# Kernel optimization log

Measured on AMD Instinct MI355X. Metric: run time of the kernel, lower is better.

Reference implementation:

```python
import jax, jax.numpy as jnp
import numpy as np
from jax import lax

EPS = 1e-12
ALPHA = 20.0
TEMP = 10.0
TAU = 0.45
LAMBDA_N = 0.3
REP_W = 0.15
MOMENTUM = 0.9
N_SINK_ITER = 3


def _norm(x):
    # F.normalize(p=2, dim=1, eps=1e-12)
    return x / jnp.maximum(jnp.linalg.norm(x, axis=-1, keepdims=True), EPS)


def sinkhorn(sim, alpha=ALPHA, n_iterations=N_SINK_ITER):
    Q = jnp.exp(alpha * sim).T  # [K, B]
    K, B = Q.shape
    Q = Q / jnp.sum(Q)
    for _ in range(n_iterations):
        Q = Q / (jnp.sum(Q, axis=1, keepdims=True) * K)
        Q = Q / (jnp.sum(Q, axis=0, keepdims=True) * B)
    return (Q * B).T  # [B, K]


def update_negative_centers(n_feats, positive_center, negative_centers):
    # all under no_grad in the original
    nf = _norm(n_feats)
    pos = _norm(positive_center)
    sim_to_pos = (nf @ pos.T)[:, 0]                       # [Nn]
    keep = sim_to_pos < 0.7
    negc = _norm(negative_centers)
    sim = nf @ negc.T                                     # [Nn, K]
    assign = jnp.argmax(sim, axis=1)
    K = negative_centers.shape[0]
    onehot = jax.nn.one_hot(assign, K, dtype=n_feats.dtype) * keep[:, None].astype(n_feats.dtype)
    counts = jnp.sum(onehot, axis=0)                      # [K]
    sums = onehot.T @ n_feats                             # [K, D] masked per-cluster sums of raw feats
    means = sums / jnp.maximum(counts[:, None], 1.0)
    new_center = _norm(means)
    lerped = negative_centers + (new_center - negative_centers) * (1.0 - MOMENTUM)
    lerped = lerped / jnp.maximum(jnp.linalg.norm(lerped, axis=1, keepdims=True), EPS)
    # update only clusters with >=3 assigned kept features (skips everything if keep.sum()==0)
    return jnp.where((counts >= 3.0)[:, None], lerped, negative_centers)


def setup_inputs() -> dict:
    key = jax.random.key(0)
    ks = jax.random.split(key, 6)
    dim, n_proxies, n_centers = 512, 1024, 4
    return {
        'p_feats': jax.random.normal(ks[0], (16384, dim), jnp.float32),
        'u_feats': jax.random.normal(ks[1], (65536, dim), jnp.float32),
        'n_feats': jax.random.normal(ks[2], (32768, dim), jnp.float32),
        'positive_center': _norm(jax.random.normal(ks[3], (1, dim), jnp.float32)),
        'proxy_u': jax.random.normal(ks[4], (n_proxies, dim), jnp.float32),
        'negative_centers': _norm(jax.random.normal(ks[5], (n_centers, dim), jnp.float32)),
    }


def reference(p_feats, u_feats, n_feats, positive_center, proxy_u, negative_centers):
    pos = lax.stop_gradient(positive_center)   # requires_grad=False param
    negc0 = lax.stop_gradient(negative_centers)  # buffer

    # l_loss: mean(1 - cos(pos, p_feats))
    dist = _norm(pos) @ _norm(p_feats).T       # [1, Np]
    l_loss = jnp.mean(1.0 - dist)

    # EMA update of negative centers (no_grad)
    negc = lax.stop_gradient(update_negative_centers(lax.stop_gradient(n_feats), pos, negc0))

    # n branch: self-distillation on negative centers
    sim_n = _norm(n_feats) @ _norm(negc).T     # [Nn, K]
    target_n = jax.nn.softmax(sim_n, axis=1)
    loss_n = -jnp.mean(jnp.sum(target_n * jax.nn.log_softmax(sim_n, axis=1), axis=1))

    # pseudo-label branch on u_feats vs negative centers (sinkhorn targets, detached)
    sim_u_neg = _norm(u_feats) @ _norm(negc).T  # [Nu, K]
    soft_assign = sinkhorn(lax.stop_gradient(sim_u_neg))
    loss_pseudo = -jnp.mean(jnp.sum(soft_assign * jax.nn.log_softmax(sim_u_neg, axis=1), axis=1))

    n_loss = (loss_n + loss_pseudo) / 2.0

    # u branch vs learnable proxies
    u_similarity = _norm(u_feats) @ _norm(proxy_u).T  # [Nu, P]
    u_target = sinkhorn(lax.stop_gradient(u_similarity))
    u_loss = -jnp.mean(jnp.sum(u_target * jax.nn.log_softmax(u_similarity * TEMP, axis=1), axis=1))

    # repulsion
    sim_np = (_norm(negc) @ _norm(pos).T)[:, 0]       # [K]
    rep_np = -jnp.mean(jnp.log(jnp.clip(1.0 - sim_np, 1e-6, None)))
    nc = _norm(negc)
    sim_nn = nc @ nc.T                                 # [K, K]
    K = negc.shape[0]
    offdiag = ~jnp.eye(K, dtype=bool)
    logs = jnp.where(offdiag, jnp.log(jnp.clip(1.0 - sim_nn, 1e-6, None)), 0.0)
    rep_nn = -jnp.sum(logs) / (K * K - K)
    repulsion_loss = rep_np + 0.1 * rep_nn

    cls_loss = TAU * l_loss + LAMBDA_N * n_loss + (0.55 - TAU) * u_loss + REP_W * repulsion_loss
    return cls_loss, l_loss, u_loss, n_loss, repulsion_loss
```

## Files before the change

kernel.cpp:

```cpp
#include <hip/hip_runtime.h>
#include <hip/hip_bf16.h>

typedef __attribute__((ext_vector_type(8))) short short8;
typedef __attribute__((ext_vector_type(8))) unsigned short ushort8;
typedef __attribute__((ext_vector_type(4))) float f32x4;

#define EPSN 1e-12f
#define GN 1024
#define GK 512

__device__ __forceinline__ float bf2f(unsigned short h) {
  union { unsigned int u; float f; } c; c.u = ((unsigned int)h) << 16; return c.f;
}
__device__ __forceinline__ unsigned short f2bf(float f) {
  union { float f; unsigned int u; } c; c.f = f;
  unsigned int u = c.u;
  return (unsigned short)((u + 0x7fffu + ((u >> 16) & 1u)) >> 16);
}
__device__ __forceinline__ float wredsum(float v) {
  v += __shfl_xor(v, 32); v += __shfl_xor(v, 16); v += __shfl_xor(v, 8);
  v += __shfl_xor(v, 4);  v += __shfl_xor(v, 2);  v += __shfl_xor(v, 1);
  return v;
}

#define GLL(g, l) __builtin_amdgcn_global_load_lds( \
    (const __attribute__((address_space(1))) unsigned int*)(g), \
    (__attribute__((address_space(3))) unsigned int*)(l), 16, 0, 0)

__global__ void k_prep(const float* __restrict__ pc, const float* __restrict__ nc,
                       float* __restrict__ pos_hat, float* __restrict__ negc0_hat) {
  int tid = threadIdx.x, lane = tid & 63, w = tid >> 6;
  const float* src = (w == 0) ? pc : (nc + (w - 1) * 512);
  float* dst = (w == 0) ? pos_hat : (negc0_hat + (w - 1) * 512);
  float4 a = *(const float4*)(src + lane * 8);
  float4 b = *(const float4*)(src + lane * 8 + 4);
  float x[8] = {a.x,a.y,a.z,a.w,b.x,b.y,b.z,b.w};
  float ss = 0.f;
  #pragma unroll
  for (int j = 0; j < 8; j++) ss += x[j]*x[j];
  ss = wredsum(ss);
  float inv = 1.f / fmaxf(sqrtf(ss), EPSN);
  #pragma unroll
  for (int j = 0; j < 8; j++) dst[lane*8+j] = x[j]*inv;
}

__global__ __launch_bounds__(256) void k_redcol(const float* __restrict__ P, float* __restrict__ R,
                                                int nrows, int ncols) {
  __shared__ float lred[64];
  int tid = threadIdx.x, lane = tid & 63, w = tid >> 6;
  int colg = blockIdx.x * 16;
  int ci = tid & 15;
  int r0 = tid >> 4;
  float s = 0.f;
  for (int r = r0; r < nrows; r += 16)
    s += P[(size_t)r * ncols + colg + ci];
  s += __shfl_xor(s, 16); s += __shfl_xor(s, 32);
  if (lane < 16) lred[w * 16 + lane] = s;
  __syncthreads();
  if (tid < 16) R[colg + tid] = lred[tid] + lred[16 + tid] + lred[32 + tid] + lred[48 + tid];
}

__global__ __launch_bounds__(256) void k_rownormP(const float* __restrict__ X,
                                                  unsigned short* __restrict__ Y,
                                                  float* __restrict__ invn, int rows) {
  int lane = threadIdx.x & 63;
  int w0 = blockIdx.x * 4 + (threadIdx.x >> 6);
  int nw = gridDim.x * 4;
  for (int row = w0; row < rows; row += nw) {
    const float* src = X + (size_t)row * 512 + lane * 8;
    float4 a = *(const float4*)src;
    float4 b = *(const float4*)(src + 4);
    float x[8] = {a.x,a.y,a.z,a.w,b.x,b.y,b.z,b.w};
    float ss = 0.f;
    #pragma unroll
    for (int j = 0; j < 8; j++) ss += x[j]*x[j];
    ss = wredsum(ss);
    float inv = 1.f / fmaxf(sqrtf(ss), EPSN);
    if (lane == 0) invn[row] = inv;
    ushort8 o;
    #pragma unroll
    for (int j = 0; j < 8; j++) o[j] = f2bf(x[j]);
    *(ushort8*)(Y + (size_t)row * 512 + lane * 8) = o;
  }
}

__global__ __launch_bounds__(256) void k_plns(const float* __restrict__ PF, const float* __restrict__ ph_g,
                                              float* __restrict__ PlossP,
                                              const float* __restrict__ NF, const float* __restrict__ nch0,
                                              float* __restrict__ inv_n, float* __restrict__ CntP,
                                              float* __restrict__ SumP) {
  __shared__ float fl[8192];
  __shared__ float cb[16];
  int tid = threadIdx.x, lane = tid & 63, w = tid >> 6;
  if (blockIdx.x < 512) {
    float ph[8];
    #pragma unroll
    for (int j = 0; j < 8; j++) ph[j] = ph_g[lane*8+j];
    float lsum = 0.f;
    int row0 = blockIdx.x * 32;
    for (int rr = w; rr < 32; rr += 4) {
      int row = row0 + rr;
      const float* src = PF + (size_t)row * 512 + lane * 8;
      float4 a = *(const float4*)src;
      float4 b = *(const float4*)(src + 4);
      float x[8] = {a.x,a.y,a.z,a.w,b.x,b.y,b.z,b.w};
      float ss = 0.f, dp = 0.f;
      #pragma unroll
      for (int j = 0; j < 8; j++) { ss += x[j]*x[j]; dp += x[j]*ph[j]; }
      ss = wredsum(ss); dp = wredsum(dp);
      if (lane == 0) lsum += dp / fmaxf(sqrtf(ss), EPSN);
    }
    if (lane == 0) cb[w] = lsum;
    __syncthreads();
    if (tid == 0) PlossP[blockIdx.x] = cb[0]+cb[1]+cb[2]+cb[3];
    return;
  }
  const int nb = blockIdx.x - 512;
  float ph[8], nh[4][8];
  #pragma unroll
  for (int j = 0; j < 8; j++) ph[j] = ph_g[lane*8+j];
  #pragma unroll
  for (int c = 0; c < 4; c++)
    #pragma unroll
    for (int j = 0; j < 8; j++) nh[c][j] = nch0[c*512 + lane*8 + j];
  float acc[4][8];
  float cnt[4] = {0.f,0.f,0.f,0.f};
  #pragma unroll
  for (int c = 0; c < 4; c++)
    #pragma unroll
    for (int j = 0; j < 8; j++) acc[c][j] = 0.f;
  int row0 = nb * 32;
  for (int rr = w; rr < 32; rr += 4) {
    int row = row0 + rr;
    const float* src = NF + (size_t)row * 512 + lane * 8;
    float4 a = *(const float4*)src;
    float4 b = *(const float4*)(src + 4);
    float x[8] = {a.x,a.y,a.z,a.w,b.x,b.y,b.z,b.w};
    float ss = 0.f, dp = 0.f, dn[4] = {0.f,0.f,0.f,0.f};
    #pragma unroll
    for (int j = 0; j < 8; j++) {
      ss += x[j]*x[j]; dp += x[j]*ph[j];
      #pragma unroll
      for (int c = 0; c < 4; c++) dn[c] += x[j]*nh[c][j];
    }
    ss = wredsum(ss); dp = wredsum(dp);
    #pragma unroll
    for (int c = 0; c < 4; c++) dn[c] = wredsum(dn[c]);
    float inv = 1.f / fmaxf(sqrtf(ss), EPSN);
    if (lane == 0) inv_n[row] = inv;
    float sp = dp * inv;
    float s0 = dn[0]*inv, s1 = dn[1]*inv, s2 = dn[2]*inv, s3 = dn[3]*inv;
    int am = 0; float best = s0;
    if (s1 > best) { best = s1; am = 1; }
    if (s2 > best) { best = s2; am = 2; }
    if (s3 > best) { best = s3; am = 3; }
    float kf = (sp < 0.7f) ? 1.f : 0.f;
    #pragma unroll
    for (int c = 0; c < 4; c++) {
      float m = (am == c) ? kf : 0.f;
      #pragma unroll
      for (int j = 0; j < 8; j++) acc[c][j] += m * x[j];
      if (lane == 0) cnt[c] += m;
    }
  }
  #pragma unroll
  for (int c = 0; c < 4; c++)
    #pragma unroll
    for (int j = 0; j < 8; j++) fl[w*2048 + c*512 + lane*8 + j] = acc[c][j];
  if (lane == 0) {
    #pragma unroll
    for (int c = 0; c < 4; c++) cb[w*4+c] = cnt[c];
  }
  __syncthreads();
  for (int q = tid; q < 2048; q += 256)
    SumP[(size_t)nb * 2048 + q] = fl[q] + fl[2048+q] + fl[4096+q] + fl[6144+q];
  if (tid < 4) CntP[nb * 4 + tid] = cb[tid] + cb[4+tid] + cb[8+tid] + cb[12+tid];
}

__global__ void k_center(const float* __restrict__ CntP, const float* __restrict__ sums,
                         const float* __restrict__ negc_raw, const float* __restrict__ pos_hat,
                         float* __restrict__ negc_hat, float* __restrict__ scal) {
  __shared__ float hbuf[2048];
  __shared__ float spn[4];
  __shared__ float snn[16];
  int tid = threadIdx.x, lane = tid & 63, c = tid >> 6;
  float cs = 0.f;
  for (int r = lane; r < 1024; r += 64) cs += CntP[r*4 + c];
  float cnt = wredsum(cs);
  float x[8], raw[8], ph[8];
  #pragma unroll
  for (int j = 0; j < 8; j++) {
    x[j] = sums[c*512 + lane*8 + j] / fmaxf(cnt, 1.f);
    raw[j] = negc_raw[c*512 + lane*8 + j];
    ph[j] = pos_hat[lane*8 + j];
  }
  float ss = 0.f;
  #pragma unroll
  for (int j = 0; j < 8; j++) ss += x[j]*x[j];
  ss = wredsum(ss);
  float n1 = fmaxf(sqrtf(ss), EPSN);
  #pragma unroll
  for (int j = 0; j < 8; j++) x[j] = raw[j] + (x[j]/n1 - raw[j]) * 0.1f;
  ss = 0.f;
  #pragma unroll
  for (int j = 0; j < 8; j++) ss += x[j]*x[j];
  ss = wredsum(ss);
  float n2 = fmaxf(sqrtf(ss), EPSN);
  bool upd = (cnt >= 3.0f);
  #pragma unroll
  for (int j = 0; j < 8; j++) x[j] = upd ? (x[j]/n2) : raw[j];
  ss = 0.f;
  #pragma unroll
  for (int j = 0; j < 8; j++) ss += x[j]*x[j];
  ss = wredsum(ss);
  float n3 = fmaxf(sqrtf(ss), EPSN);
  float dp = 0.f;
  #pragma unroll
  for (int j = 0; j < 8; j++) {
    x[j] = x[j] / n3;
    negc_hat[c*512 + lane*8 + j] = x[j];
    hbuf[c*512 + lane*8 + j] = x[j];
    dp += x[j] * ph[j];
  }
  dp = wredsum(dp);
  if (lane == 0) spn[c] = dp;
  __syncthreads();
  float d4[4] = {0.f,0.f,0.f,0.f};
  #pragma unroll
  for (int c2 = 0; c2 < 4; c2++) {
    float d = 0.f;
    #pragma unroll
    for (int j = 0; j < 8; j++) d += x[j] * hbuf[c2*512 + lane*8 + j];
    d4[c2] = wredsum(d);
  }
  if (lane == 0) {
    #pragma unroll
    for (int c2 = 0; c2 < 4; c2++) snn[c*4 + c2] = d4[c2];
  }
  __syncthreads();
  if (tid == 0) {
    float rep_np = 0.f;
    for (int i = 0; i < 4; i++) rep_np += logf(fmaxf(1.f - spn[i], 1e-6f));
    rep_np = -rep_np * 0.25f;
    float rep_nn = 0.f;
    for (int i = 0; i < 4; i++)
      for (int j2 = 0; j2 < 4; j2++)
        if (i != j2) rep_nn += logf(fmaxf(1.f - snn[i*4+j2], 1e-6f));
    rep_nn = -rep_nn / 12.f;
    scal[4] = rep_np + 0.1f * rep_nn;
  }
}

__global__ __launch_bounds__(256) void k_nlup(const float* __restrict__ NF, const float* __restrict__ inv_n,
                                              const float* __restrict__ nch, float* __restrict__ NlossP,
                                              const float* __restrict__ U, float* __restrict__ SU,
                                              float* __restrict__ UPp, unsigned short* __restrict__ Uh,
                                              float* __restrict__ invU) {
  __shared__ float sh[16];
  int tid = threadIdx.x, lane = tid & 63, w = tid >> 6;
  float nh[4][8];
  #pragma unroll
  for (int c = 0; c < 4; c++)
    #pragma unroll
    for (int j = 0; j < 8; j++) nh[c][j] = nch[c*512 + lane*8 + j];
  if (blockIdx.x < 1024) {
    float lsum = 0.f;
    int row0 = blockIdx.x * 32;
    for (int rr = w; rr < 32; rr += 4) {
      int row = row0 + rr;
      const float* src = NF + (size_t)row * 512 + lane * 8;
      float4 a = *(const float4*)src;
      float4 b = *(const float4*)(src + 4);
      float x[8] = {a.x,a.y,a.z,a.w,b.x,b.y,b.z,b.w};
      float dn[4] = {0.f,0.f,0.f,0.f};
      #pragma unroll
      for (int j = 0; j < 8; j++)
        #pragma unroll
        for (int c = 0; c < 4; c++) dn[c] += x[j]*nh[c][j];
      #pragma unroll
      for (int c = 0; c < 4; c++) dn[c] = wredsum(dn[c]);
      if (lane == 0) {
        float inv = inv_n[row];
        float s0 = dn[0]*inv, s1 = dn[1]*inv, s2 = dn[2]*inv, s3 = dn[3]*inv;
        float mx = fmaxf(fmaxf(s0,s1), fmaxf(s2,s3));
        float e0 = __expf(s0-mx), e1 = __expf(s1-mx), e2 = __expf(s2-mx), e3 = __expf(s3-mx);
        float Z = e0+e1+e2+e3;
        lsum += (mx + logf(Z)) - (e0*s0+e1*s1+e2*s2+e3*s3)/Z;
      }
    }
    if (lane == 0) sh[w] = lsum;
    __syncthreads();
    if (tid == 0) NlossP[blockIdx.x] = sh[0]+sh[1]+sh[2]+sh[3];
    return;
  }
  const int ub = blockIdx.x - 1024;
  float eacc[4] = {0.f,0.f,0.f,0.f};
  int row0 = ub * 32;
  for (int rr = w; rr < 32; rr += 4) {
    int row = row0 + rr;
    const float* src = U + (size_t)row * 512 + lane * 8;
    float4 a = *(const float4*)src;
    float4 b = *(const float4*)(src + 4);
    float x[8] = {a.x,a.y,a.z,a.w,b.x,b.y,b.z,b.w};
    float ss = 0.f, dn[4] = {0.f,0.f,0.f,0.f};
    #pragma unroll
    for (int j = 0; j < 8; j++) {
      ss += x[j]*x[j];
      #pragma unroll
      for (int c = 0; c < 4; c++) dn[c] += x[j]*nh[c][j];
    }
    ss = wredsum(ss);
    #pragma unroll
    for (int c = 0; c < 4; c++) dn[c] = wredsum(dn[c]);
    float inv = 1.f / fmaxf(sqrtf(ss), EPSN);
    ushort8 o;
    #pragma unroll
    for (int j = 0; j < 8; j++) o[j] = f2bf(x[j]);
    *(ushort8*)(Uh + (size_t)row * 512 + lane * 8) = o;
    if (lane == 0) {
      invU[row] = inv;
      float4 sv; sv.x = dn[0]*inv; sv.y = dn[1]*inv; sv.z = dn[2]*inv; sv.w = dn[3]*inv;
      *(float4*)(SU + (size_t)row * 4) = sv;
      eacc[0] += __expf(20.f*sv.x); eacc[1] += __expf(20.f*sv.y);
      eacc[2] += __expf(20.f*sv.z); eacc[3] += __expf(20.f*sv.w);
    }
  }
  if (lane == 0) {
    #pragma unroll
    for (int c = 0; c < 4; c++) sh[w*4+c] = eacc[c];
  }
  __syncthreads();
  if (tid < 4) UPp[ub * 4 + tid] = sh[tid] + sh[4+tid] + sh[8+tid] + sh[12+tid];
}

__global__ __launch_bounds__(256) void k_psink(const float* __restrict__ SU, const float* __restrict__ Pin,
                                               int n_in, float* __restrict__ Pout,
                                               float* __restrict__ PLout, int mode) {
  __shared__ float lr[16];
  int tid = threadIdx.x, lane = tid & 63, w = tid >> 6;
  float i0 = 0.f, i1 = 0.f, i2 = 0.f, i3 = 0.f;
  for (int r = tid; r < n_in; r += 256) {
    float4 v = *(const float4*)(Pin + (size_t)r * 4);
    i0 += v.x; i1 += v.y; i2 += v.z; i3 += v.w;
  }
  i0 = wredsum(i0); i1 = wredsum(i1); i2 = wredsum(i2); i3 = wredsum(i3);
  if (lane == 0) { lr[w*4+0] = i0; lr[w*4+1] = i1; lr[w*4+2] = i2; lr[w*4+3] = i3; }
  __syncthreads();
  float R0 = lr[0]+lr[4]+lr[8]+lr[12];
  float R1_ = lr[1]+lr[5]+lr[9]+lr[13];
  float R2_ = lr[2]+lr[6]+lr[10]+lr[14];
  float R3_ = lr[3]+lr[7]+lr[11]+lr[15];
  float r0 = 1.f/(4.f*R0), r1 = 1.f/(4.f*R1_), r2 = 1.f/(4.f*R2_), r3 = 1.f/(4.f*R3_);
  float a0 = 0.f, a1 = 0.f, a2 = 0.f, a3 = 0.f, lsum = 0.f;
  int row = blockIdx.x * blockDim.x + threadIdx.x;
  {
    float4 s = *(const float4*)(SU + (size_t)row * 4);
    float x0 = __expf(20.f*s.x), x1 = __expf(20.f*s.y);
    float x2 = __expf(20.f*s.z), x3 = __expf(20.f*s.w);
    float E0 = x0*r0, E1 = x1*r1, E2 = x2*r2, E3 = x3*r3;
    float cf = 1.f / ((E0+E1+E2+E3) * 65536.f);
    if (mode == 1) { a0 = x0*cf; a1 = x1*cf; a2 = x2*cf; a3 = x3*cf; }
    else {
      float term = (E0*s.x + E1*s.y + E2*s.z + E3*s.w) * 65536.f * cf;
      float mx = fmaxf(fmaxf(s.x,s.y), fmaxf(s.z,s.w));
      float z = __expf(s.x-mx)+__expf(s.y-mx)+__expf(s.z-mx)+__expf(s.w-mx);
      lsum = (mx + logf(z)) - term;
    }
  }
  __syncthreads();
  if (mode == 1) {
    a0 = wredsum(a0); a1 = wredsum(a1); a2 = wredsum(a2); a3 = wredsum(a3);
    if (lane == 0) { lr[w*4+0] = a0; lr[w*4+1] = a1; lr[w*4+2] = a2; lr[w*4+3] = a3; }
    __syncthreads();
    if (tid < 4) Pout[blockIdx.x * 4 + tid] = lr[tid] + lr[4+tid] + lr[8+tid] + lr[12+tid];
  } else {
    lsum = wredsum(lsum);
    if (lane == 0) lr[w] = lsum;
    __syncthreads();
    if (tid == 0) PLout[blockIdx.x] = lr[0]+lr[1]+lr[2]+lr[3];
  }
}

__global__ __launch_bounds__(512) void k_gemm(const unsigned short* __restrict__ A,
                                              const unsigned short* __restrict__ B,
                                              const float* __restrict__ invU,
                                              const float* __restrict__ invP,
                                              unsigned short* __restrict__ S,
                                              float* __restrict__ R1) {
  __shared__ unsigned short lAB[24576];
  __shared__ float red[1024];
  unsigned short* lA = lAB;
  unsigned short* lB = lAB + 16384;
  const int swz = (blockIdx.x & 7) * 256 + (blockIdx.x >> 3);
  const int rowblk = swz >> 3, colblk = swz & 7;
  const int tid = threadIdx.x, lane = tid & 63;
  const int wid = tid >> 6, wm = wid >> 1, wn = wid & 1;
  f32x4 acc[4][4];
  #pragma unroll
  for (int m = 0; m < 4; m++)
    #pragma unroll
    for (int n = 0; n < 4; n++) acc[m][n] = (f32x4){0.f,0.f,0.f,0.f};
  const unsigned short* Ag = A + (size_t)rowblk * 256 * GK;
  const unsigned short* Bg = B + (size_t)colblk * 128 * GK;
  const int r0 = tid >> 3;
  const int c0 = ((tid & 7) ^ (r0 & 7)) * 8;
  for (int kt = 0; kt < GK; kt += 64) {
    #pragma unroll
    for (int i = 0; i < 4; i++)
      GLL(Ag + (size_t)(r0 + i*64) * GK + kt + c0, lA + (i*512 + tid) * 8);
    #pragma unroll
    for (int i = 0; i < 2; i++)
      GLL(Bg + (size_t)(r0 + i*64) * GK + kt + c0, lB + (i*512 + tid) * 8);
    __syncthreads();
    #pragma unroll
    for (int kk = 0; kk < 2; kk++) {
      short8 af[4], bf[4];
      #pragma unroll
      for (int m = 0; m < 4; m++) {
        int rowA = wm*64 + m*16 + (lane & 15);
        int ch = ((kk*4 + (lane >> 4)) ^ (rowA & 7)) * 8;
        af[m] = *(const short8*)(lA + rowA * 64 + ch);
      }
      #pragma unroll
      for (int n = 0; n < 4; n++) {
        int rowB = wn*64 + n*16 + (lane & 15);
        int ch = ((kk*4 + (lane >> 4)) ^ (rowB & 7)) * 8;
        bf[n] = *(const short8*)(lB + rowB * 64 + ch);
      }
      #pragma unroll
      for (int m = 0; m < 4; m++)
        #pragma unroll
        for (int n = 0; n < 4; n++)
          acc[m][n] = __builtin_amdgcn_mfma_f32_16x16x32_bf16(af[m], bf[n], acc[m][n], 0, 0, 0);
    }
    __syncthreads();
  }
  unsigned short* lC = lAB;
  float racc[16];
  #pragma unroll
  for (int j = 0; j < 16; j++) racc[j] = 0.f;
  const size_t outbase = (size_t)rowblk * 256 * GN + (size_t)colblk * 128;
  const int ch8 = lane & 7, rsub = lane >> 3;
  #pragma unroll
  for (int h = 0; h < 2; h++) {
    if ((wm >> 1) == h) {
      #pragma unroll
      for (int m = 0; m < 4; m++)
        #pragma unroll
        for (int n = 0; n < 4; n++) {
          int col = wn*64 + n*16 + (lane & 15);
          float ip = invP[colblk * 128 + col];
          #pragma unroll
          for (int r = 0; r < 4; r++) {
            int lr2 = (wm & 1)*64 + m*16 + ((lane >> 4) << 2) + r;
            float iu = invU[rowblk * 256 + h*128 + lr2];
            lC[lr2 * 136 + col] = f2bf(acc[m][n][r] * iu * ip);
          }
        }
    }
    __syncthreads();
    #pragma unroll
    for (int it = 0; it < 2; it++) {
      int lr2 = it*64 + wid*8 + rsub;
      int grow = h*128 + lr2;
      ushort8 v0 = *(const ushort8*)(lC + lr2 * 136 + ch8 * 8);
      ushort8 v1 = *(const ushort8*)(lC + lr2 * 136 + 64 + ch8 * 8);
      *(short8*)(S + outbase + (size_t)grow * GN + ch8 * 8) = (short8)v0;
      *(short8*)(S + outbase + (size_t)grow * GN + 64 + ch8 * 8) = (short8)v1;
      #pragma unroll
      for (int j = 0; j < 8; j++) {
        racc[j]     += __expf(20.f * bf2f(v0[j]));
        racc[8 + j] += __expf(20.f * bf2f(v1[j]));
      }
    }
    __syncthreads();
  }
  #pragma unroll
  for (int j = 0; j < 16; j++) {
    racc[j] += __shfl_xor(racc[j], 8);
    racc[j] += __shfl_xor(racc[j], 16);
    racc[j] += __shfl_xor(racc[j], 32);
  }
  if (lane < 8) {
    #pragma unroll
    for (int j = 0; j < 8; j++) {
      red[wid * 128 + lane * 8 + j]      = racc[j];
      red[wid * 128 + 64 + lane * 8 + j] = racc[8 + j];
    }
  }
  __syncthreads();
  if (tid < 128) {
    float s8 = 0.f;
    #pragma unroll
    for (int i = 0; i < 8; i++) s8 += red[i * 128 + tid];
    int gcol = colblk * 128 + tid;
    int q = (gcol & 15) * 64 + (gcol >> 4);
    atomicAdd(&R1[q], s8);
  }
}

__global__ __launch_bounds__(256) void k_sink1(const unsigned short* __restrict__ S,
                                               const float* __restrict__ Rin,
                                               float* __restrict__ Pout) {
  __shared__ float lds[4096];
  int tid = threadIdx.x, lane = tid & 63, w = tid >> 6;
  float rj[16];
  #pragma unroll
  for (int j = 0; j < 16; j++) rj[j] = 1.f / (1024.f * Rin[j*64 + lane]);
  float acc[16];
  #pragma unroll
  for (int j = 0; j < 16; j++) acc[j] = 0.f;
  int row0 = blockIdx.x * 32;
  for (int rr = w; rr < 16; rr += 4) {
    const unsigned short* SrA = S + (size_t)(row0 + rr) * 1024 + lane * 16;
    const unsigned short* SrB = S + (size_t)(row0 + rr + 16) * 1024 + lane * 16;
    ushort8 a0 = *(const ushort8*)SrA, a1 = *(const ushort8*)(SrA + 8);
    ushort8 b0 = *(const ushort8*)SrB, b1 = *(const ushort8*)(SrB + 8);
    float XA[16], XB[16];
    float csA = 0.f, csB = 0.f;
    #pragma unroll
    for (int j = 0; j < 8; j++) {
      XA[j]   = __expf(20.f * bf2f(a0[j]));
      XA[8+j] = __expf(20.f * bf2f(a1[j]));
      XB[j]   = __expf(20.f * bf2f(b0[j]));
      XB[8+j] = __expf(20.f * bf2f(b1[j]));
    }
    #pragma unroll
    for (int j = 0; j < 16; j++) { csA += XA[j]*rj[j]; csB += XB[j]*rj[j]; }
    #pragma unroll
    for (int d = 32; d >= 1; d >>= 1) {
      csA += __shfl_xor(csA, d);
      csB += __shfl_xor(csB, d);
    }
    float cfA = 1.f / (csA * 65536.f), cfB = 1.f / (csB * 65536.f);
    #pragma unroll
    for (int j = 0; j < 16; j++) acc[j] += XA[j]*cfA + XB[j]*cfB;
  }
  #pragma unroll
  for (int j = 0; j < 16; j++) lds[w*1024 + lane + 64*j] = acc[j];
  __syncthreads();
  for (int q = tid; q < 1024; q += 256)
    Pout[(size_t)blockIdx.x * 1024 + q] = lds[q] + lds[1024+q] + lds[2048+q] + lds[3072+q];
}

__global__ __launch_bounds__(256) void k_sinkL(const unsigned short* __restrict__ S,
                                               const float* __restrict__ Rin,
                                               float* __restrict__ LPout) {
  __shared__ float lr[4];
  int tid = threadIdx.x, lane = tid & 63, w = tid >> 6;
  float rj[16];
  #pragma unroll
  for (int j = 0; j < 16; j++) rj[j] = 1.f / (1024.f * Rin[j*64 + lane]);
  float lsum = 0.f;
  int row0 = blockIdx.x * 32;
  for (int rr = w; rr < 16; rr += 4) {
    const unsigned short* SrA = S + (size_t)(row0 + rr) * 1024 + lane * 16;
    const unsigned short* SrB = S + (size_t)(row0 + rr + 16) * 1024 + lane * 16;
    ushort8 a0 = *(const ushort8*)SrA, a1 = *(const ushort8*)(SrA + 8);
    ushort8 b0 = *(const ushort8*)SrB, b1 = *(const ushort8*)(SrB + 8);
    float sA[16], sB[16], yA[16], yB[16];
    #pragma unroll
    for (int j = 0; j < 8; j++) {
      sA[j] = bf2f(a0[j]); sA[8+j] = bf2f(a1[j]);
      sB[j] = bf2f(b0[j]); sB[8+j] = bf2f(b1[j]);
    }
    #pragma unroll
    for (int j = 0; j < 16; j++) { yA[j] = __expf(10.f*sA[j]); yB[j] = __expf(10.f*sB[j]); }
    float csA = 0.f, csB = 0.f, tA = 0.f, tB = 0.f, YA = 0.f, YB = 0.f;
    #pragma unroll
    for (int j = 0; j < 16; j++) {
      float xa = yA[j]*yA[j]*rj[j];
      float xb = yB[j]*yB[j]*rj[j];
      csA += xa; tA += xa*sA[j]; YA += yA[j];
      csB += xb; tB += xb*sB[j]; YB += yB[j];
    }
    #pragma unroll
    for (int d = 32; d >= 1; d >>= 1) {
      csA += __shfl_xor(csA, d); csB += __shfl_xor(csB, d);
      tA  += __shfl_xor(tA, d);  tB  += __shfl_xor(tB, d);
      YA  += __shfl_xor(YA, d);  YB  += __shfl_xor(YB, d);
    }
    if (lane == 0)
      lsum += (logf(YA) - 10.f*tA/csA) + (logf(YB) - 10.f*tB/csB);
  }
  if (lane == 0) lr[w] = lsum;
  __syncthreads();
  if (tid == 0) LPout[blockIdx.x] = lr[0]+lr[1]+lr[2]+lr[3];
}

__global__ __launch_bounds__(256) void k_final(const float* __restrict__ scal,
                                               const float* __restrict__ PlossP,
                                               const float* __restrict__ NlossP,
                                               const float* __restrict__ PLp,
                                               const float* __restrict__ SLp,
                                               float* __restrict__ out) {
  __shared__ float lr[4];
  int tid = threadIdx.x, lane = tid & 63, w = tid >> 6;
  float tots[4];
  const float* arrs[4] = {PlossP, NlossP, PLp, SLp};
  const int ns[4] = {512, 1024, 256, 2048};
  for (int k = 0; k < 4; k++) {
    float s = 0.f;
    for (int i = tid; i < ns[k]; i += 256) s += arrs[k][i];
    s = wredsum(s);
    __syncthreads();
    if (lane == 0) lr[w] = s;
    __syncthreads();
    tots[k] = lr[0]+lr[1]+lr[2]+lr[3];
  }
  if (tid == 0) {
    float l   = 1.f - tots[0] / 16384.f;
    float ln  = tots[1] / 32768.f;
    float lp  = tots[2] / 65536.f;
    float ul  = tots[3] / 65536.f;
    float rep = scal[4];
    float nl  = 0.5f * (ln + lp);
    float cls = 0.45f*l + 0.3f*nl + 0.1f*ul + 0.15f*rep;
    out[0] = cls;
    out[1] = l;
    out[2] = ul;
    out[3] = nl;
    out[4] = rep;
  }
}

extern "C" void kernel_launch(void* const* d_in, const int* in_sizes, int n_in,
                              void* d_out, int out_size, void* d_ws, size_t ws_size,
                              hipStream_t stream) {
  const float* PF = (const float*)d_in[0];
  const float* UF = (const float*)d_in[1];
  const float* NF = (const float*)d_in[2];
  const float* PC = (const float*)d_in[3];
  const float* PU = (const float*)d_in[4];
  const float* NC = (const float*)d_in[5];

  char* ws = (char*)d_ws;
  const size_t WS_REQUIRED = 202736768ULL;
  if (ws_size < WS_REQUIRED) return;

  float* R1     = (float*)(ws + 0);
  float* R2     = (float*)(ws + 4096);
  float* R3     = (float*)(ws + 8192);
  float* scal   = (float*)(ws + 12288);
  float* sums   = (float*)(ws + 12416);
  float* invP   = (float*)(ws + 20608);
  float* UPp    = (float*)(ws + 24704);
  float* PPpA   = (float*)(ws + 57472);
  float* PPpB   = (float*)(ws + 61568);
  float* PLp    = (float*)(ws + 65664);
  float* PlossP = (float*)(ws + 66688);
  float* NlossP = (float*)(ws + 68736);
  float* pos_hat   = (float*)(ws + 81024);
  float* negc0_hat = (float*)(ws + 83072);
  float* negc_hat  = (float*)(ws + 91264);
  float* invU      = (float*)(ws + 99456);
  float* SU    = (float*)(ws + 361600);
  unsigned short* Ph = (unsigned short*)(ws + 361600);
  float* SumP = (float*)(ws + 1410176);
  unsigned short* Uh = (unsigned short*)(ws + 1410176);
  float* SPp  = (float*)(ws + 1410176);
  float* SLp  = (float*)(ws + 9798784);
  float* CntP = (float*)(ws + 9806976);
  unsigned short* S = (unsigned short*)(ws + 68519040);
  float* inv_n = (float*)(ws + 68519040);

  hipMemsetAsync(ws, 0, 4096, stream);

  k_prep<<<1, 320, 0, stream>>>(PC, NC, pos_hat, negc0_hat);
  k_plns<<<1536, 256, 0, stream>>>(PF, pos_hat, PlossP, NF, negc0_hat, inv_n, CntP, SumP);
  k_redcol<<<128, 256, 0, stream>>>(SumP, sums, 1024, 2048);
  k_center<<<1, 256, 0, stream>>>(CntP, sums, NC, pos_hat, negc_hat, scal);
  k_nlup<<<3072, 256, 0, stream>>>(NF, inv_n, negc_hat, NlossP, UF, SU, UPp, Uh, invU);

  k_psink<<<256, 256, 0, stream>>>(SU, UPp, 2048, PPpA, nullptr, 1);
  k_psink<<<256, 256, 0, stream>>>(SU, PPpA, 256, PPpB, nullptr, 1);
  k_psink<<<256, 256, 0, stream>>>(SU, PPpB, 256, nullptr, PLp, 2);

  k_rownormP<<<32, 256, 0, stream>>>(PU, Ph, invP, 1024);

  k_gemm<<<2048, 512, 0, stream>>>(Uh, Ph, invU, invP, S, R1);
  k_sink1<<<2048, 256, 0, stream>>>(S, R1, SPp);
  k_redcol<<<64, 256, 0, stream>>>(SPp, R2, 2048, 1024);
  k_sink1<<<2048, 256, 0, stream>>>(S, R2, SPp);
  k_redcol<<<64, 256, 0, stream>>>(SPp, R3, 2048, 1024);
  k_sinkL<<<2048, 256, 0, stream>>>(S, R3, SLp);

  k_final<<<1, 256, 0, stream>>>(scal, PlossP, NlossP, PLp, SLp, (float*)d_out);
}
```

Baseline: 412.2 us.

## Double-buffer GEMM k-loop with async global-to-LDS prefetch

Restructures the bf16 GEMM main loop to use two LDS buffers with K-tile 32 instead of a single buffer with K-tile 64. Loads for tile t+2 are issued right after computing tile t, with explicit vmcnt waits and raw barriers, so global loads overlap MFMA work. The swizzle and fragment offsets are recomputed for the narrower tile and hoisted out of the loop. The cost is more loop iterations and barriers, and a dependence on hand-placed waitcnt ordering being correct.

```diff
diff --git a/kernel.cpp b/kernel.cpp
--- a/kernel.cpp
+++ b/kernel.cpp
@@ -389,8 +389,6 @@
                                               float* __restrict__ R1) {
   __shared__ unsigned short lAB[24576];
   __shared__ float red[1024];
-  unsigned short* lA = lAB;
-  unsigned short* lB = lAB + 16384;
   const int swz = (blockIdx.x & 7) * 256 + (blockIdx.x >> 3);
   const int rowblk = swz >> 3, colblk = swz & 7;
   const int tid = threadIdx.x, lane = tid & 63;
@@ -402,39 +400,70 @@
     for (int n = 0; n < 4; n++) acc[m][n] = (f32x4){0.f,0.f,0.f,0.f};
   const unsigned short* Ag = A + (size_t)rowblk * 256 * GK;
   const unsigned short* Bg = B + (size_t)colblk * 128 * GK;
-  const int r0 = tid >> 3;
-  const int c0 = ((tid & 7) ^ (r0 & 7)) * 8;
-  for (int kt = 0; kt < GK; kt += 64) {
-    #pragma unroll
-    for (int i = 0; i < 4; i++)
-      GLL(Ag + (size_t)(r0 + i*64) * GK + kt + c0, lA + (i*512 + tid) * 8);
-    #pragma unroll
-    for (int i = 0; i < 2; i++)
-      GLL(Bg + (size_t)(r0 + i*64) * GK + kt + c0, lB + (i*512 + tid) * 8);
-    __syncthreads();
-    #pragma unroll
-    for (int kk = 0; kk < 2; kk++) {
-      short8 af[4], bf[4];
-      #pragma unroll
-      for (int m = 0; m < 4; m++) {
-        int rowA = wm*64 + m*16 + (lane & 15);
-        int ch = ((kk*4 + (lane >> 4)) ^ (rowA & 7)) * 8;
-        af[m] = *(const short8*)(lA + rowA * 64 + ch);
-      }
-      #pragma unroll
-      for (int n = 0; n < 4; n++) {
-        int rowB = wn*64 + n*16 + (lane & 15);
-        int ch = ((kk*4 + (lane >> 4)) ^ (rowB & 7)) * 8;
-        bf[n] = *(const short8*)(lB + rowB * 64 + ch);
-      }
-      #pragma unroll
-      for (int m = 0; m < 4; m++)
-        #pragma unroll
-        for (int n = 0; n < 4; n++)
-          acc[m][n] = __builtin_amdgcn_mfma_f32_16x16x32_bf16(af[m], bf[n], acc[m][n], 0, 0, 0);
-    }
-    __syncthreads();
-  }
+  const int sr = tid >> 2;
+  const int sc = ((tid & 3) ^ ((sr >> 1) & 3)) * 8;
+  int rA[4], cAo[4], rB[4], cBo[4];
+  #pragma unroll
+  for (int m = 0; m < 4; m++) {
+    rA[m] = wm*64 + m*16 + (lane & 15);
+    cAo[m] = rA[m]*32 + (((lane >> 4) ^ ((rA[m] >> 1) & 3)) * 8);
+  }
+  #pragma unroll
+  for (int n = 0; n < 4; n++) {
+    rB[n] = wn*64 + n*16 + (lane & 15);
+    cBo[n] = 8192 + rB[n]*32 + (((lane >> 4) ^ ((rB[n] >> 1) & 3)) * 8);
+  }
+  #pragma unroll
+  for (int t = 0; t < 2; t++) {
+    unsigned short* nb = lAB + t * 12288;
+    const int kt = t * 32;
+    GLL(Ag + (size_t)sr * GK + kt + sc,         nb + tid * 8);
+    GLL(Ag + (size_t)(sr + 128) * GK + kt + sc, nb + (512 + tid) * 8);
+    GLL(Bg + (size_t)sr * GK + kt + sc,         nb + (1024 + tid) * 8);
+  }
+  for (int t = 0; t < 15; t++) {
+    asm volatile("s_waitcnt vmcnt(3)" ::: "memory");
+    __builtin_amdgcn_s_barrier();
+    asm volatile("" ::: "memory");
+    const unsigned short* cb = lAB + (t & 1) * 12288;
+    short8 af[4], bf[4];
+    #pragma unroll
+    for (int m = 0; m < 4; m++) af[m] = *(const short8*)(cb + cAo[m]);
+    #pragma unroll
+    for (int n = 0; n < 4; n++) bf[n] = *(const short8*)(cb + cBo[n]);
+    #pragma unroll
+    for (int m = 0; m < 4; m++)
+      #pragma unroll
+      for (int n = 0; n < 4; n++)
+        acc[m][n] = __builtin_amdgcn_mfma_f32_16x16x32_bf16(af[m], bf[n], acc[m][n], 0, 0, 0);
+    asm volatile("" ::: "memory");
+    __builtin_amdgcn_s_barrier();
+    asm volatile("" ::: "memory");
+    if (t < 14) {
+      unsigned short* nb = lAB + (t & 1) * 12288;
+      const int kt = (t + 2) * 32;
+      GLL(Ag + (size_t)sr * GK + kt + sc,         nb + tid * 8);
+      GLL(Ag + (size_t)(sr + 128) * GK + kt + sc, nb + (512 + tid) * 8);
+      GLL(Bg + (size_t)sr * GK + kt + sc,         nb + (1024 + tid) * 8);
+    }
+  }
+  asm volatile("s_waitcnt vmcnt(0)" ::: "memory");
+  __builtin_amdgcn_s_barrier();
+  asm volatile("" ::: "memory");
+  {
+    const unsigned short* cb = lAB + 12288;
+    short8 af[4], bf[4];
+    #pragma unroll
+    for (int m = 0; m < 4; m++) af[m] = *(const short8*)(cb + cAo[m]);
+    #pragma unroll
+    for (int n = 0; n < 4; n++) bf[n] = *(const short8*)(cb + cBo[n]);
+    #pragma unroll
+    for (int m = 0; m < 4; m++)
+      #pragma unroll
+      for (int n = 0; n < 4; n++)
+        acc[m][n] = __builtin_amdgcn_mfma_f32_16x16x32_bf16(af[m], bf[n], acc[m][n], 0, 0, 0);
+  }
+  __syncthreads();
   unsigned short* lC = lAB;
   float racc[16];
   #pragma unroll
```

Result: slower. 421.1 us (+2.2%).
